# Optimization experiments

Measured on AMD Instinct MI355X. Metric: run time of the kernel, lower is better.

Reference implementation:

```python
import jax, jax.numpy as jnp
import numpy as np

EPS = 1e-12  # F.normalize eps
NUM_CLASSES = 80


def _l2_normalize(x, axis):
    # matches torch F.normalize: x / max(||x||_2, eps)
    n = jnp.sqrt(jnp.sum(x * x, axis=axis, keepdims=True))
    return x / jnp.maximum(n, EPS)


def setup_inputs() -> dict:
    key = jax.random.key(0)
    k1, k2, k3, k4 = jax.random.split(key, 4)
    B, C, H, W = 16, 256, 128, 128
    N = NUM_CLASSES
    features = jax.random.normal(k1, (B, C, H, W), dtype=jnp.float32)
    centroids = jax.random.normal(k2, (N, C), dtype=jnp.float32)
    fc_w = jax.random.normal(k3, (C, C, 1, 1), dtype=jnp.float32) * 0.02
    fc_b = jax.random.normal(k4, (C,), dtype=jnp.float32) * 0.01
    return {"features": features, "centroids": centroids, "fc_w": fc_w, "fc_b": fc_b}


def reference(features, centroids, fc_w, fc_b):
    N = centroids.shape[0]
    # cosine similarity to class centroids: [B, N, H, W]
    sim = jnp.einsum('bchw,nc->bnhw', _l2_normalize(features, axis=1),
                     _l2_normalize(centroids, axis=1))
    # hard one-hot assignment along class dim (scatter of argmax)
    idx = jnp.argmax(sim, axis=1)                              # [B, H, W]
    mask = jax.nn.one_hot(idx, N, axis=1, dtype=features.dtype)  # [B, N, H, W]
    # per-image, per-class mean feature (gather/blend)
    sum_x = jnp.einsum('bnhw,bchw->bnc', mask, features)       # [B, N, C]
    count = jnp.sum(mask, axis=(2, 3))[:, :, None]             # [B, N, 1]
    cent = sum_x / jnp.maximum(count, 1.0)
    delta = jnp.einsum('bnhw,bnc->bchw', mask, cent) - features
    alpha = jnp.exp(-jnp.mean(jnp.square(delta), axis=1, keepdims=True))  # [B,1,H,W]
    x = features + alpha * delta
    # 1x1 conv == channel matmul
    out = jnp.einsum('bchw,oc->bohw', x, fc_w[:, :, 0, 0]) + fc_b[None, :, None, None]
    return jax.nn.relu(out)
```

## Files before the change

kernel.cpp:

```cpp
#include <hip/hip_runtime.h>


typedef __bf16 bf16x8 __attribute__((ext_vector_type(8)));
typedef float  f32x4  __attribute__((ext_vector_type(4)));
typedef unsigned char u8;

__device__ __forceinline__ unsigned short f2b(float f) {
  unsigned u = __float_as_uint(f);
  return (unsigned short)((u + 0x7fffu + ((u >> 16) & 1u)) >> 16);
}
__device__ __forceinline__ float b2f(unsigned short s) {
  return __uint_as_float((unsigned)s << 16);
}

__global__ __launch_bounds__(256) void k0_cnorm(const float* __restrict__ cent,
                                                float* __restrict__ cnT,
                                                int* __restrict__ cntg) {
  int n = blockIdx.x, t = threadIdx.x;
  if (t < 16) cntg[n * 16 + t] = 0;
  float v = cent[n * 256 + t];
  float s = v * v;
  #pragma unroll
  for (int o = 32; o > 0; o >>= 1) s += __shfl_down(s, o, 64);
  __shared__ float red[4];
  if ((t & 63) == 0) red[t >> 6] = s;
  __syncthreads();
  float tot = red[0] + red[1] + red[2] + red[3];
  float dn = fmaxf(sqrtf(tot), 1e-12f);
  cnT[t * 80 + n] = v / dn;
}

__global__ __launch_bounds__(256) void k0_wprep(const float* __restrict__ fcw,
                                                unsigned short* __restrict__ wks,
                                                float* __restrict__ wt) {
  int o = blockIdx.x, c = threadIdx.x;
  float w = fcw[o * 256 + c];
  wt[c * 256 + o] = w;
  wks[((c >> 5) * 256 + o) * 32 + (c & 31)] = f2b(w);
}

__global__ __launch_bounds__(256) void k1_argmax(const float* __restrict__ feat,
                                                 const float* __restrict__ cnT,
                                                 u8* __restrict__ idxb,
                                                 float* __restrict__ fsqg,
                                                 int* __restrict__ cntg) {
  __shared__ int lh[80];
  int t = threadIdx.x;
  if (t < 80) lh[t] = 0;
  __syncthreads();
  int b = blockIdx.x >> 6;
  int pi = ((blockIdx.x & 63) << 8) | t;
  const float* fb = feat + (size_t)b * 256 * 16384 + pi;
  float g[80];
  #pragma unroll
  for (int n = 0; n < 80; ++n) g[n] = 0.f;
  float fsq = 0.f;
  #pragma unroll 4
  for (int c = 0; c < 256; ++c) {
    float v = fb[(size_t)c * 16384];
    fsq = fmaf(v, v, fsq);
    const float* cr = cnT + c * 80;
    #pragma unroll
    for (int n = 0; n < 80; ++n) g[n] = fmaf(v, cr[n], g[n]);
  }
  float best = g[0]; int bi = 0;
  #pragma unroll
  for (int n = 1; n < 80; ++n) if (g[n] > best) { best = g[n]; bi = n; }
  idxb[b * 16384 + pi] = (u8)bi;
  fsqg[b * 16384 + pi] = fsq;
  atomicAdd(&lh[bi], 1);
  __syncthreads();
  if (t < 80) atomicAdd(&cntg[b * 80 + t], lh[t]);
}

__global__ __launch_bounds__(256) void k1b_gemm(const float* __restrict__ feat,
                                                const u8* __restrict__ idxb,
                                                unsigned short* __restrict__ sumxp) {
  int bid = blockIdx.x;
  int kp = bid & 3, ns = (bid >> 2) & 7, b = bid >> 5;
  int t = threadIdx.x, wv = t >> 6, ln = t & 63, lo = ln & 15, hi = ln >> 4;
  int nt = wv & 1;
  int m0 = (wv >> 1) ? 3 : 0, nm = (wv >> 1) ? 2 : 3;
  int c = ns * 32 + nt * 16 + lo;
  const float* fp = feat + (((size_t)b * 256 + c) * 16384 + kp * 4096 + hi * 8);
  const u8* ip = idxb + b * 16384 + kp * 4096 + hi * 8;
  f32x4 acc[3];
  f32x4 zz = {0.f, 0.f, 0.f, 0.f};
  acc[0] = zz; acc[1] = zz; acc[2] = zz;
  for (int ks = 0; ks < 128; ++ks) {
    float4 v0 = *(const float4*)(fp + ks * 32);
    float4 v1 = *(const float4*)(fp + ks * 32 + 4);
    union { unsigned short u[8]; bf16x8 v; } bb;
    bb.u[0] = f2b(v0.x); bb.u[1] = f2b(v0.y); bb.u[2] = f2b(v0.z); bb.u[3] = f2b(v0.w);
    bb.u[4] = f2b(v1.x); bb.u[5] = f2b(v1.y); bb.u[6] = f2b(v1.z); bb.u[7] = f2b(v1.w);
    uint2 iv = *(const uint2*)(ip + ks * 32);
    int id[8];
    #pragma unroll
    for (int j = 0; j < 4; ++j) { id[j] = (iv.x >> (8 * j)) & 255; id[4 + j] = (iv.y >> (8 * j)) & 255; }
    #pragma unroll
    for (int mi = 0; mi < 3; ++mi) {
      if (mi >= nm) break;
      int row = (m0 + mi) * 16 + lo;
      union { unsigned short u[8]; bf16x8 v; } ma;
      #pragma unroll
      for (int j = 0; j < 8; ++j) ma.u[j] = (id[j] == row) ? (unsigned short)0x3F80 : (unsigned short)0;
      acc[mi] = __builtin_amdgcn_mfma_f32_16x16x32_bf16(ma.v, bb.v, acc[mi], 0, 0, 0);
    }
  }
  #pragma unroll
  for (int mi = 0; mi < 3; ++mi) {
    if (mi >= nm) break;
    #pragma unroll
    for (int r = 0; r < 4; ++r) {
      int cls = (m0 + mi) * 16 + hi * 4 + r;
      sumxp[(((size_t)kp * 16 + b) * 80 + cls) * 256 + ns * 32 + nt * 16 + lo] = f2b(acc[mi][r]);
    }
  }
}

__global__ __launch_bounds__(256) void k2_cent(const unsigned short* __restrict__ sumxp,
                                               const int* __restrict__ cntg,
                                               const float* __restrict__ wt,
                                               unsigned short* __restrict__ centf,
                                               float* __restrict__ csqg,
                                               float* __restrict__ chatg) {
  int bn = blockIdx.x; int t = threadIdx.x;
  float dn = fmaxf((float)cntg[bn], 1.0f);
  float s = 0.f;
  #pragma unroll
  for (int kp = 0; kp < 4; ++kp)
    s += b2f(sumxp[((size_t)kp * 1280 + bn) * 256 + t]);
  float cv = s / dn;
  __shared__ float cl[256];
  __shared__ float red[4];
  cl[t] = cv;
  centf[(size_t)bn * 256 + t] = f2b(cv);
  float q = cv * cv;
  #pragma unroll
  for (int o = 32; o > 0; o >>= 1) q += __shfl_down(q, o, 64);
  if ((t & 63) == 0) red[t >> 6] = q;
  __syncthreads();
  if (t == 0) csqg[bn] = red[0] + red[1] + red[2] + red[3];
  float acc = 0.f;
  #pragma unroll 4
  for (int c = 0; c < 256; ++c) acc = fmaf(wt[c * 256 + t], cl[c], acc);
  chatg[(size_t)bn * 256 + t] = acc;
}

__global__ __launch_bounds__(512) void k3b_gemm(const float* __restrict__ feat,
    const u8* __restrict__ idxb, const float* __restrict__ fsqg,
    const float* __restrict__ csqg, const unsigned short* __restrict__ centf,
    const float* __restrict__ chatg, const unsigned short* __restrict__ wks,
    const float* __restrict__ fcb, float* __restrict__ out) {
  __shared__ alignas(16) unsigned short featT[64 * 264];
  __shared__ float alphal[64];
  const int t = threadIdx.x;
  const int w = t >> 6, ln = t & 63, lo = ln & 15, hi = ln >> 4;

  bf16x8 wf[2][8];
  #pragma unroll
  for (int ml = 0; ml < 2; ++ml)
    #pragma unroll
    for (int ks = 0; ks < 8; ++ks)
      wf[ml][ks] = *(const bf16x8*)&wks[((size_t)ks * 256 + (w * 2 + ml) * 16 + lo) * 32 + hi * 8];
  f32x4 bias2[2];
  #pragma unroll
  for (int ml = 0; ml < 2; ++ml)
    bias2[ml] = *(const f32x4*)&fcb[w * 32 + ml * 16 + hi * 4];

  for (int rep = 0; rep < 2; ++rep) {
    int tile = blockIdx.x * 2 + rep;
    int b = tile >> 8;
    int p0 = (tile & 255) << 6;

    {
      int pl = t & 63, cph = t >> 6;
      const float* fb = feat + ((size_t)b * 256 + cph * 32) * 16384 + p0 + pl;
      #pragma unroll
      for (int jj = 0; jj < 4; ++jj) {
        union { unsigned short u[8]; uint4 q; } pk;
        #pragma unroll
        for (int e = 0; e < 8; ++e) pk.u[e] = f2b(fb[(size_t)(jj * 8 + e) * 16384]);
        *(uint4*)&featT[pl * 264 + cph * 32 + jj * 8] = pk.q;
      }
    }
    __syncthreads();

    {
      int p = t >> 3, sub = t & 7;
      int cid = idxb[b * 16384 + p0 + p];
      const unsigned short* cw = centf + ((size_t)b * 80 + cid) * 256 + sub * 32;
      const unsigned short* fr = &featT[p * 264 + sub * 32];
      float sel = 0.f;
      #pragma unroll
      for (int j = 0; j < 4; ++j) {
        uint4 cc = *(const uint4*)&cw[j * 8];
        uint4 ff = *(const uint4*)&fr[j * 8];
        sel = fmaf(b2f((unsigned short)(ff.x & 0xffff)), b2f((unsigned short)(cc.x & 0xffff)), sel);
        sel = fmaf(b2f((unsigned short)(ff.x >> 16)),    b2f((unsigned short)(cc.x >> 16)),    sel);
        sel = fmaf(b2f((unsigned short)(ff.y & 0xffff)), b2f((unsigned short)(cc.y & 0xffff)), sel);
        sel = fmaf(b2f((unsigned short)(ff.y >> 16)),    b2f((unsigned short)(cc.y >> 16)),    sel);
        sel = fmaf(b2f((unsigned short)(ff.z & 0xffff)), b2f((unsigned short)(cc.z & 0xffff)), sel);
        sel = fmaf(b2f((unsigned short)(ff.z >> 16)),    b2f((unsigned short)(cc.z >> 16)),    sel);
        sel = fmaf(b2f((unsigned short)(ff.w & 0xffff)), b2f((unsigned short)(cc.w & 0xffff)), sel);
        sel = fmaf(b2f((unsigned short)(ff.w >> 16)),    b2f((unsigned short)(cc.w >> 16)),    sel);
      }
      sel += __shfl_xor(sel, 1, 64);
      sel += __shfl_xor(sel, 2, 64);
      sel += __shfl_xor(sel, 4, 64);
      if (sub == 0) {
        float fsq = fsqg[b * 16384 + p0 + p];
        float msq = (csqg[b * 80 + cid] - 2.f * sel + fsq) * (1.f / 256.f);
        alphal[p] = expf(-msq);
      }
    }

    f32x4 acc[2][4];
    f32x4 zz = {0.f, 0.f, 0.f, 0.f};
    #pragma unroll
    for (int ml = 0; ml < 2; ++ml)
      #pragma unroll
      for (int pt = 0; pt < 4; ++pt) acc[ml][pt] = zz;

    #pragma unroll
    for (int ks = 0; ks < 8; ++ks) {
      bf16x8 bfr[4];
      #pragma unroll
      for (int pt = 0; pt < 4; ++pt)
        bfr[pt] = *(const bf16x8*)&featT[(pt * 16 + lo) * 264 + ks * 32 + hi * 8];
      #pragma unroll
      for (int ml = 0; ml < 2; ++ml)
        #pragma unroll
        for (int pt = 0; pt < 4; ++pt)
          acc[ml][pt] = __builtin_amdgcn_mfma_f32_16x16x32_bf16(wf[ml][ks], bfr[pt], acc[ml][pt], 0, 0, 0);
    }
    __syncthreads();

    #pragma unroll
    for (int pt = 0; pt < 4; ++pt) {
      int pl = pt * 16 + lo;
      int p = p0 + pl;
      float a = alphal[pl];
      float om = 1.f - a;
      int cid = idxb[b * 16384 + p];
      const float* crow = chatg + ((size_t)b * 80 + cid) * 256;
      #pragma unroll
      for (int ml = 0; ml < 2; ++ml) {
        int o0 = w * 32 + ml * 16 + hi * 4;
        float4 c4 = *(const float4*)&crow[o0];
        size_t ob = ((size_t)b * 256 + o0) * 16384 + p;
        out[ob            ] = fmaxf(fmaf(a, c4.x, om * acc[ml][pt][0]) + bias2[ml][0], 0.f);
        out[ob + 16384    ] = fmaxf(fmaf(a, c4.y, om * acc[ml][pt][1]) + bias2[ml][1], 0.f);
        out[ob + 2 * 16384] = fmaxf(fmaf(a, c4.z, om * acc[ml][pt][2]) + bias2[ml][2], 0.f);
        out[ob + 3 * 16384] = fmaxf(fmaf(a, c4.w, om * acc[ml][pt][3]) + bias2[ml][3], 0.f);
      }
    }
    __syncthreads();
  }
}

extern "C" void kernel_launch(void* const* d_in, const int* in_sizes, int n_in,
                              void* d_out, int out_size, void* d_ws, size_t ws_size,
                              hipStream_t stream) {
  (void)in_sizes; (void)n_in; (void)out_size; (void)ws_size;
  const float* feat = (const float*)d_in[0];
  const float* cent = (const float*)d_in[1];
  const float* fcw  = (const float*)d_in[2];
  const float* fcb  = (const float*)d_in[3];
  float* out = (float*)d_out;
  char* ws = (char*)d_ws;
  float* cnT             = (float*)(ws);
  float* wt              = (float*)(ws + 81920);
  unsigned short* wks    = (unsigned short*)(ws + 344064);
  unsigned short* centf  = (unsigned short*)(ws + 475136);
  u8*    idxb            = (u8*)(ws + 1130496);
  float* fsq             = (float*)(ws + 1392640);
  int*   cntg            = (int*)(ws + 2441216);
  float* csq             = (float*)(ws + 2446336);
  float* chat            = (float*)(ws + 2451456);
  unsigned short* sumxp  = (unsigned short*)(ws + 3762176);

  k0_cnorm<<<80, 256, 0, stream>>>(cent, cnT, cntg);
  k0_wprep<<<256, 256, 0, stream>>>(fcw, wks, wt);
  k1_argmax<<<1024, 256, 0, stream>>>(feat, cnT, idxb, fsq, cntg);
  k1b_gemm<<<512, 256, 0, stream>>>(feat, idxb, sumxp);
  k2_cent<<<1280, 256, 0, stream>>>(sumxp, cntg, wt, centf, csq, chat);
  k3b_gemm<<<2048, 512, 0, stream>>>(feat, idxb, fsq, csq, centf, chat, wks, fcb, out);
}
```

Before: 465.6 us.

## Fuse argmax with class-sum GEMM and double-buffer feature tiles in final GEMM

```diff
diff --git a/kernel.cpp b/kernel.cpp
--- a/kernel.cpp
+++ b/kernel.cpp
@@ -32,93 +32,107 @@
 
 __global__ __launch_bounds__(256) void k0_wprep(const float* __restrict__ fcw,
                                                 unsigned short* __restrict__ wks,
-                                                float* __restrict__ wt) {
+                                                float* __restrict__ wt,
+                                                int* __restrict__ sumxi) {
   int o = blockIdx.x, c = threadIdx.x;
   float w = fcw[o * 256 + c];
   wt[c * 256 + o] = w;
   wks[((c >> 5) * 256 + o) * 32 + (c & 31)] = f2b(w);
-}
-
-__global__ __launch_bounds__(256) void k1_argmax(const float* __restrict__ feat,
-                                                 const float* __restrict__ cnT,
-                                                 u8* __restrict__ idxb,
-                                                 float* __restrict__ fsqg,
-                                                 int* __restrict__ cntg) {
+  for (int i = o * 256 + c; i < 16 * 80 * 256; i += 65536) sumxi[i] = 0;
+}
+
+__global__ __launch_bounds__(256) void k1f(const float* __restrict__ feat,
+                                           const float* __restrict__ cnT,
+                                           u8* __restrict__ idxb,
+                                           float* __restrict__ fsqg,
+                                           int* __restrict__ cntg,
+                                           int* __restrict__ sumxi) {
+  __shared__ alignas(8) u8 idxl[256];
   __shared__ int lh[80];
-  int t = threadIdx.x;
+  const int bid = blockIdx.x;
+  const int b = bid >> 5, kp = bid & 31;
+  const int t = threadIdx.x, wv = t >> 6, ln = t & 63, lo = ln & 15, hi = ln >> 4;
+
+  f32x4 acc[5][4];
+  f32x4 zz = {0.f, 0.f, 0.f, 0.f};
+  #pragma unroll
+  for (int mt = 0; mt < 5; ++mt)
+    #pragma unroll
+    for (int nt = 0; nt < 4; ++nt) acc[mt][nt] = zz;
   if (t < 80) lh[t] = 0;
-  __syncthreads();
-  int b = blockIdx.x >> 6;
-  int pi = ((blockIdx.x & 63) << 8) | t;
-  const float* fb = feat + (size_t)b * 256 * 16384 + pi;
-  float g[80];
-  #pragma unroll
-  for (int n = 0; n < 80; ++n) g[n] = 0.f;
-  float fsq = 0.f;
-  #pragma unroll 4
-  for (int c = 0; c < 256; ++c) {
-    float v = fb[(size_t)c * 16384];
-    fsq = fmaf(v, v, fsq);
-    const float* cr = cnT + c * 80;
-    #pragma unroll
-    for (int n = 0; n < 80; ++n) g[n] = fmaf(v, cr[n], g[n]);
+
+  for (int cc = 0; cc < 2; ++cc) {
+    const int px0 = kp * 512 + cc * 256;
+    __syncthreads();
+
+    const float* fb = feat + (size_t)b * 256 * 16384 + px0 + t;
+    float g[80];
+    #pragma unroll
+    for (int n = 0; n < 80; ++n) g[n] = 0.f;
+    float fsq = 0.f;
+    #pragma unroll 4
+    for (int c = 0; c < 256; ++c) {
+      float v = fb[(size_t)c * 16384];
+      fsq = fmaf(v, v, fsq);
+      const float* cr = cnT + c * 80;
+      #pragma unroll
+      for (int n = 0; n < 80; ++n) g[n] = fmaf(v, cr[n], g[n]);
+    }
+    float best = g[0]; int bi = 0;
+    #pragma unroll
+    for (int n = 1; n < 80; ++n) if (g[n] > best) { best = g[n]; bi = n; }
+    idxb[b * 16384 + px0 + t] = (u8)bi;
+    fsqg[b * 16384 + px0 + t] = fsq;
+    idxl[t] = (u8)bi;
+    atomicAdd(&lh[bi], 1);
+    __syncthreads();
+
+    const int chb = wv * 64;
+    #pragma unroll 2
+    for (int ks = 0; ks < 8; ++ks) {
+      uint2 iv = *(const uint2*)&idxl[ks * 32 + hi * 8];
+      int id[8];
+      #pragma unroll
+      for (int j = 0; j < 4; ++j) { id[j] = (iv.x >> (8 * j)) & 255; id[4 + j] = (iv.y >> (8 * j)) & 255; }
+      bf16x8 bfr[4];
+      #pragma unroll
+      for (int nt = 0; nt < 4; ++nt) {
+        const float* bp = feat + ((size_t)b * 256 + chb + nt * 16 + lo) * 16384 + px0 + ks * 32 + hi * 8;
+        float4 v0 = *(const float4*)bp;
+        float4 v1 = *(const float4*)(bp + 4);
+        union { unsigned short u[8]; bf16x8 v; } bb;
+        bb.u[0] = f2b(v0.x); bb.u[1] = f2b(v0.y); bb.u[2] = f2b(v0.z); bb.u[3] = f2b(v0.w);
+        bb.u[4] = f2b(v1.x); bb.u[5] = f2b(v1.y); bb.u[6] = f2b(v1.z); bb.u[7] = f2b(v1.w);
+        bfr[nt] = bb.v;
+      }
+      #pragma unroll
+      for (int mt = 0; mt < 5; ++mt) {
+        int row = mt * 16 + lo;
+        union { unsigned short u[8]; bf16x8 v; } ma;
+        #pragma unroll
+        for (int j = 0; j < 8; ++j) ma.u[j] = (id[j] == row) ? (unsigned short)0x3F80 : (unsigned short)0;
+        #pragma unroll
+        for (int nt = 0; nt < 4; ++nt)
+          acc[mt][nt] = __builtin_amdgcn_mfma_f32_16x16x32_bf16(ma.v, bfr[nt], acc[mt][nt], 0, 0, 0);
+      }
+    }
   }
-  float best = g[0]; int bi = 0;
-  #pragma unroll
-  for (int n = 1; n < 80; ++n) if (g[n] > best) { best = g[n]; bi = n; }
-  idxb[b * 16384 + pi] = (u8)bi;
-  fsqg[b * 16384 + pi] = fsq;
-  atomicAdd(&lh[bi], 1);
   __syncthreads();
   if (t < 80) atomicAdd(&cntg[b * 80 + t], lh[t]);
-}
-
-__global__ __launch_bounds__(256) void k1b_gemm(const float* __restrict__ feat,
-                                                const u8* __restrict__ idxb,
-                                                unsigned short* __restrict__ sumxp) {
-  int bid = blockIdx.x;
-  int kp = bid & 3, ns = (bid >> 2) & 7, b = bid >> 5;
-  int t = threadIdx.x, wv = t >> 6, ln = t & 63, lo = ln & 15, hi = ln >> 4;
-  int nt = wv & 1;
-  int m0 = (wv >> 1) ? 3 : 0, nm = (wv >> 1) ? 2 : 3;
-  int c = ns * 32 + nt * 16 + lo;
-  const float* fp = feat + (((size_t)b * 256 + c) * 16384 + kp * 4096 + hi * 8);
-  const u8* ip = idxb + b * 16384 + kp * 4096 + hi * 8;
-  f32x4 acc[3];
-  f32x4 zz = {0.f, 0.f, 0.f, 0.f};
-  acc[0] = zz; acc[1] = zz; acc[2] = zz;
-  for (int ks = 0; ks < 128; ++ks) {
-    float4 v0 = *(const float4*)(fp + ks * 32);
-    float4 v1 = *(const float4*)(fp + ks * 32 + 4);
-    union { unsigned short u[8]; bf16x8 v; } bb;
-    bb.u[0] = f2b(v0.x); bb.u[1] = f2b(v0.y); bb.u[2] = f2b(v0.z); bb.u[3] = f2b(v0.w);
-    bb.u[4] = f2b(v1.x); bb.u[5] = f2b(v1.y); bb.u[6] = f2b(v1.z); bb.u[7] = f2b(v1.w);
-    uint2 iv = *(const uint2*)(ip + ks * 32);
-    int id[8];
-    #pragma unroll
-    for (int j = 0; j < 4; ++j) { id[j] = (iv.x >> (8 * j)) & 255; id[4 + j] = (iv.y >> (8 * j)) & 255; }
-    #pragma unroll
-    for (int mi = 0; mi < 3; ++mi) {
-      if (mi >= nm) break;
-      int row = (m0 + mi) * 16 + lo;
-      union { unsigned short u[8]; bf16x8 v; } ma;
-      #pragma unroll
-      for (int j = 0; j < 8; ++j) ma.u[j] = (id[j] == row) ? (unsigned short)0x3F80 : (unsigned short)0;
-      acc[mi] = __builtin_amdgcn_mfma_f32_16x16x32_bf16(ma.v, bb.v, acc[mi], 0, 0, 0);
-    }
-  }
-  #pragma unroll
-  for (int mi = 0; mi < 3; ++mi) {
-    if (mi >= nm) break;
-    #pragma unroll
-    for (int r = 0; r < 4; ++r) {
-      int cls = (m0 + mi) * 16 + hi * 4 + r;
-      sumxp[(((size_t)kp * 16 + b) * 80 + cls) * 256 + ns * 32 + nt * 16 + lo] = f2b(acc[mi][r]);
-    }
-  }
-}
-
-__global__ __launch_bounds__(256) void k2_cent(const unsigned short* __restrict__ sumxp,
+  #pragma unroll
+  for (int mt = 0; mt < 5; ++mt)
+    #pragma unroll
+    for (int nt = 0; nt < 4; ++nt)
+      #pragma unroll
+      for (int r = 0; r < 4; ++r) {
+        int cls = mt * 16 + hi * 4 + r;
+        int ch = wv * 64 + nt * 16 + lo;
+        atomicAdd(&sumxi[((size_t)b * 80 + cls) * 256 + ch],
+                  __float2int_rn(acc[mt][nt][r] * 8192.f));
+      }
+}
+
+__global__ __launch_bounds__(256) void k2_cent(const int* __restrict__ sumxi,
                                                const int* __restrict__ cntg,
                                                const float* __restrict__ wt,
                                                unsigned short* __restrict__ centf,
@@ -126,11 +140,7 @@
                                                float* __restrict__ chatg) {
   int bn = blockIdx.x; int t = threadIdx.x;
   float dn = fmaxf((float)cntg[bn], 1.0f);
-  float s = 0.f;
-  #pragma unroll
-  for (int kp = 0; kp < 4; ++kp)
-    s += b2f(sumxp[((size_t)kp * 1280 + bn) * 256 + t]);
-  float cv = s / dn;
+  float cv = (float)sumxi[(size_t)bn * 256 + t] * (1.0f / 8192.0f) / dn;
   __shared__ float cl[256];
   __shared__ float red[4];
   cl[t] = cv;
@@ -152,10 +162,11 @@
     const float* __restrict__ csqg, const unsigned short* __restrict__ centf,
     const float* __restrict__ chatg, const unsigned short* __restrict__ wks,
     const float* __restrict__ fcb, float* __restrict__ out) {
-  __shared__ alignas(16) unsigned short featT[64 * 264];
+  __shared__ alignas(16) unsigned short featT[2][64 * 264];
   __shared__ float alphal[64];
   const int t = threadIdx.x;
   const int w = t >> 6, ln = t & 63, lo = ln & 15, hi = ln >> 4;
+  const int pl = ln, cph = w;
 
   bf16x8 wf[2][8];
   #pragma unroll
@@ -168,29 +179,40 @@
   for (int ml = 0; ml < 2; ++ml)
     bias2[ml] = *(const f32x4*)&fcb[w * 32 + ml * 16 + hi * 4];
 
-  for (int rep = 0; rep < 2; ++rep) {
-    int tile = blockIdx.x * 2 + rep;
-    int b = tile >> 8;
-    int p0 = (tile & 255) << 6;
-
-    {
-      int pl = t & 63, cph = t >> 6;
-      const float* fb = feat + ((size_t)b * 256 + cph * 32) * 16384 + p0 + pl;
-      #pragma unroll
-      for (int jj = 0; jj < 4; ++jj) {
-        union { unsigned short u[8]; uint4 q; } pk;
-        #pragma unroll
-        for (int e = 0; e < 8; ++e) pk.u[e] = f2b(fb[(size_t)(jj * 8 + e) * 16384]);
-        *(uint4*)&featT[pl * 264 + cph * 32 + jj * 8] = pk.q;
-      }
-    }
+  const int tile0 = blockIdx.x * 8;
+  {
+    int b = tile0 >> 8, p0 = (tile0 & 255) << 6;
+    const float* fb = feat + ((size_t)b * 256 + cph * 32) * 16384 + p0 + pl;
+    #pragma unroll
+    for (int jj = 0; jj < 4; ++jj) {
+      union { unsigned short u[8]; uint4 q; } pk;
+      #pragma unroll
+      for (int e = 0; e < 8; ++e) pk.u[e] = f2b(fb[(size_t)(jj * 8 + e) * 16384]);
+      *(uint4*)&featT[0][pl * 264 + cph * 32 + jj * 8] = pk.q;
+    }
+  }
+
+  float nxv[32];
+  for (int rep = 0; rep < 8; ++rep) {
+    const int cur = rep & 1;
+    const int tile = tile0 + rep;
+    const int b = tile >> 8, p0 = (tile & 255) << 6;
+
     __syncthreads();
+
+    if (rep < 7) {
+      int t2 = tile + 1;
+      int b2 = t2 >> 8, p02 = (t2 & 255) << 6;
+      const float* fb2 = feat + ((size_t)b2 * 256 + cph * 32) * 16384 + p02 + pl;
+      #pragma unroll
+      for (int e = 0; e < 32; ++e) nxv[e] = fb2[(size_t)e * 16384];
+    }
 
     {
       int p = t >> 3, sub = t & 7;
       int cid = idxb[b * 16384 + p0 + p];
       const unsigned short* cw = centf + ((size_t)b * 80 + cid) * 256 + sub * 32;
-      const unsigned short* fr = &featT[p * 264 + sub * 32];
+      const unsigned short* fr = &featT[cur][p * 264 + sub * 32];
       float sel = 0.f;
       #pragma unroll
       for (int j = 0; j < 4; ++j) {
@@ -227,7 +249,7 @@
       bf16x8 bfr[4];
       #pragma unroll
       for (int pt = 0; pt < 4; ++pt)
-        bfr[pt] = *(const bf16x8*)&featT[(pt * 16 + lo) * 264 + ks * 32 + hi * 8];
+        bfr[pt] = *(const bf16x8*)&featT[cur][(pt * 16 + lo) * 264 + ks * 32 + hi * 8];
       #pragma unroll
       for (int ml = 0; ml < 2; ++ml)
         #pragma unroll
@@ -238,9 +260,9 @@
 
     #pragma unroll
     for (int pt = 0; pt < 4; ++pt) {
-      int pl = pt * 16 + lo;
-      int p = p0 + pl;
-      float a = alphal[pl];
+      int plx = pt * 16 + lo;
+      int p = p0 + plx;
+      float a = alphal[plx];
       float om = 1.f - a;
       int cid = idxb[b * 16384 + p];
       const float* crow = chatg + ((size_t)b * 80 + cid) * 256;
@@ -255,7 +277,16 @@
         out[ob + 3 * 16384] = fmaxf(fmaf(a, c4.w, om * acc[ml][pt][3]) + bias2[ml][3], 0.f);
       }
     }
-    __syncthreads();
+
+    if (rep < 7) {
+      #pragma unroll
+      for (int jj = 0; jj < 4; ++jj) {
+        union { unsigned short u[8]; uint4 q; } pk;
+        #pragma unroll
+        for (int e = 0; e < 8; ++e) pk.u[e] = f2b(nxv[jj * 8 + e]);
+        *(uint4*)&featT[cur ^ 1][pl * 264 + cph * 32 + jj * 8] = pk.q;
+      }
+    }
   }
 }
 
@@ -278,12 +309,11 @@
   int*   cntg            = (int*)(ws + 2441216);
   float* csq             = (float*)(ws + 2446336);
   float* chat            = (float*)(ws + 2451456);
-  unsigned short* sumxp  = (unsigned short*)(ws + 3762176);
+  int*   sumxi           = (int*)(ws + 3762176);
 
   k0_cnorm<<<80, 256, 0, stream>>>(cent, cnT, cntg);
-  k0_wprep<<<256, 256, 0, stream>>>(fcw, wks, wt);
-  k1_argmax<<<1024, 256, 0, stream>>>(feat, cnT, idxb, fsq, cntg);
-  k1b_gemm<<<512, 256, 0, stream>>>(feat, idxb, sumxp);
-  k2_cent<<<1280, 256, 0, stream>>>(sumxp, cntg, wt, centf, csq, chat);
-  k3b_gemm<<<2048, 512, 0, stream>>>(feat, idxb, fsq, csq, centf, chat, wks, fcb, out);
-}
+  k0_wprep<<<256, 256, 0, stream>>>(fcw, wks, wt, sumxi);
+  k1f<<<512, 256, 0, stream>>>(feat, cnT, idxb, fsq, cntg, sumxi);
+  k2_cent<<<1280, 256, 0, stream>>>(sumxi, cntg, wt, centf, csq, chat);
+  k3b_gemm<<<512, 512, 0, stream>>>(feat, idxb, fsq, csq, centf, chat, wks, fcb, out);
+}
```

New measurement: 485.5 us. 1.04x slower.

## Double-buffer feature tiles and prefetch next tile in persistent GEMM kernel

Applied to the files above, without the earlier changes.

```diff
diff --git a/kernel.cpp b/kernel.cpp
--- a/kernel.cpp
+++ b/kernel.cpp
@@ -152,10 +152,11 @@
     const float* __restrict__ csqg, const unsigned short* __restrict__ centf,
     const float* __restrict__ chatg, const unsigned short* __restrict__ wks,
     const float* __restrict__ fcb, float* __restrict__ out) {
-  __shared__ alignas(16) unsigned short featT[64 * 264];
+  __shared__ alignas(16) unsigned short featT[2][64 * 264];
   __shared__ float alphal[64];
   const int t = threadIdx.x;
   const int w = t >> 6, ln = t & 63, lo = ln & 15, hi = ln >> 4;
+  const int pl = ln, cph = w;
 
   bf16x8 wf[2][8];
   #pragma unroll
@@ -168,29 +169,40 @@
   for (int ml = 0; ml < 2; ++ml)
     bias2[ml] = *(const f32x4*)&fcb[w * 32 + ml * 16 + hi * 4];
 
-  for (int rep = 0; rep < 2; ++rep) {
-    int tile = blockIdx.x * 2 + rep;
-    int b = tile >> 8;
-    int p0 = (tile & 255) << 6;
-
-    {
-      int pl = t & 63, cph = t >> 6;
-      const float* fb = feat + ((size_t)b * 256 + cph * 32) * 16384 + p0 + pl;
-      #pragma unroll
-      for (int jj = 0; jj < 4; ++jj) {
-        union { unsigned short u[8]; uint4 q; } pk;
-        #pragma unroll
-        for (int e = 0; e < 8; ++e) pk.u[e] = f2b(fb[(size_t)(jj * 8 + e) * 16384]);
-        *(uint4*)&featT[pl * 264 + cph * 32 + jj * 8] = pk.q;
-      }
-    }
+  const int tile0 = blockIdx.x * 8;
+  {
+    int b = tile0 >> 8, p0 = (tile0 & 255) << 6;
+    const float* fb = feat + ((size_t)b * 256 + cph * 32) * 16384 + p0 + pl;
+    #pragma unroll
+    for (int jj = 0; jj < 4; ++jj) {
+      union { unsigned short u[8]; uint4 q; } pk;
+      #pragma unroll
+      for (int e = 0; e < 8; ++e) pk.u[e] = f2b(fb[(size_t)(jj * 8 + e) * 16384]);
+      *(uint4*)&featT[0][pl * 264 + cph * 32 + jj * 8] = pk.q;
+    }
+  }
+
+  float nxv[32];
+  for (int rep = 0; rep < 8; ++rep) {
+    const int cur = rep & 1;
+    const int tile = tile0 + rep;
+    const int b = tile >> 8, p0 = (tile & 255) << 6;
+
     __syncthreads();
+
+    if (rep < 7) {
+      int t2 = tile + 1;
+      int b2 = t2 >> 8, p02 = (t2 & 255) << 6;
+      const float* fb2 = feat + ((size_t)b2 * 256 + cph * 32) * 16384 + p02 + pl;
+      #pragma unroll
+      for (int e = 0; e < 32; ++e) nxv[e] = fb2[(size_t)e * 16384];
+    }
 
     {
       int p = t >> 3, sub = t & 7;
       int cid = idxb[b * 16384 + p0 + p];
       const unsigned short* cw = centf + ((size_t)b * 80 + cid) * 256 + sub * 32;
-      const unsigned short* fr = &featT[p * 264 + sub * 32];
+      const unsigned short* fr = &featT[cur][p * 264 + sub * 32];
       float sel = 0.f;
       #pragma unroll
       for (int j = 0; j < 4; ++j) {
@@ -227,7 +239,7 @@
       bf16x8 bfr[4];
       #pragma unroll
       for (int pt = 0; pt < 4; ++pt)
-        bfr[pt] = *(const bf16x8*)&featT[(pt * 16 + lo) * 264 + ks * 32 + hi * 8];
+        bfr[pt] = *(const bf16x8*)&featT[cur][(pt * 16 + lo) * 264 + ks * 32 + hi * 8];
       #pragma unroll
       for (int ml = 0; ml < 2; ++ml)
         #pragma unroll
@@ -238,9 +250,9 @@
 
     #pragma unroll
     for (int pt = 0; pt < 4; ++pt) {
-      int pl = pt * 16 + lo;
-      int p = p0 + pl;
-      float a = alphal[pl];
+      int plx = pt * 16 + lo;
+      int p = p0 + plx;
+      float a = alphal[plx];
       float om = 1.f - a;
       int cid = idxb[b * 16384 + p];
       const float* crow = chatg + ((size_t)b * 80 + cid) * 256;
@@ -255,7 +267,16 @@
         out[ob + 3 * 16384] = fmaxf(fmaf(a, c4.w, om * acc[ml][pt][3]) + bias2[ml][3], 0.f);
       }
     }
-    __syncthreads();
+
+    if (rep < 7) {
+      #pragma unroll
+      for (int jj = 0; jj < 4; ++jj) {
+        union { unsigned short u[8]; uint4 q; } pk;
+        #pragma unroll
+        for (int e = 0; e < 8; ++e) pk.u[e] = f2b(nxv[jj * 8 + e]);
+        *(uint4*)&featT[cur ^ 1][pl * 264 + cph * 32 + jj * 8] = pk.q;
+      }
+    }
   }
 }
 
@@ -285,5 +306,5 @@
   k1_argmax<<<1024, 256, 0, stream>>>(feat, cnT, idxb, fsq, cntg);
   k1b_gemm<<<512, 256, 0, stream>>>(feat, idxb, sumxp);
   k2_cent<<<1280, 256, 0, stream>>>(sumxp, cntg, wt, centf, csq, chat);
-  k3b_gemm<<<2048, 512, 0, stream>>>(feat, idxb, fsq, csq, centf, chat, wks, fcb, out);
-}
+  k3b_gemm<<<512, 512, 0, stream>>>(feat, idxb, fsq, csq, centf, chat, wks, fcb, out);
+}
```

Result: faster. 447.8 us (-3.8%).
